# Performance work log

Hardware: AMD Instinct MI355X
Metric: run time of the kernel (lower is better)

## Reference

```python
import jax, jax.numpy as jnp
import numpy as np

NUM_HEADS = 12

def setup_inputs() -> dict:
    key = jax.random.key(0)
    k1, k2, k3 = jax.random.split(key, 3)
    B, N, C = 2, 4096, 768
    x = jax.random.normal(k1, (B, N, C), dtype=jnp.float32)
    w_qkv = jax.random.normal(k2, (C, 3 * C), dtype=jnp.float32) * 0.02
    b_qkv = jnp.zeros((3 * C,), dtype=jnp.float32)
    w_proj = jax.random.normal(k3, (C, C), dtype=jnp.float32) * 0.02
    b_proj = jnp.zeros((C,), dtype=jnp.float32)
    return {"x": x, "w_qkv": w_qkv, "b_qkv": b_qkv, "w_proj": w_proj, "b_proj": b_proj}

def reference(x, w_qkv, b_qkv, w_proj, b_proj):
    B, N, C = x.shape
    H = NUM_HEADS
    D = C // H
    # fused QKV projection: [B,N,3C] -> [B,N,3,H,D] -> [3,B,H,N,D]
    qkv = (x @ w_qkv + b_qkv).reshape(B, N, 3, H, D).transpose(2, 0, 3, 1, 4)
    q, k, v = qkv[0], qkv[1], qkv[2]
    # unnormalized (softmax-free) attention, same op order as the torch module
    attn = jnp.einsum('bhnd,bhmd->bhnm', q, k) / jnp.sqrt(jnp.float32(D))  # [B,H,N,N]
    out = jnp.einsum('bhnm,bhmd->bhnd', attn, v)  # [B,H,N,D]
    out = out.transpose(0, 2, 1, 3).reshape(B, N, C)
    return out @ w_proj + b_proj
```

## Files before the change

kernel.cpp:

```cpp
#include <hip/hip_runtime.h>

typedef unsigned short ushort_t;
typedef __bf16 bf16_t;
typedef __attribute__((ext_vector_type(8))) bf16_t bf16x8;
typedef __attribute__((ext_vector_type(4))) float f32x4;

__device__ __forceinline__ ushort_t f2bf(float f) {
  unsigned int u = __builtin_bit_cast(unsigned int, f);
  u += 0x7FFFu + ((u >> 16) & 1u);
  return (ushort_t)(u >> 16);
}

__device__ __forceinline__ float bf2f(ushort_t s) {
  return __builtin_bit_cast(float, (unsigned int)s << 16);
}

__device__ __forceinline__ f32x4 mfma16(bf16x8 a, bf16x8 b, f32x4 c) {
  return __builtin_amdgcn_mfma_f32_16x16x32_bf16(a, b, c, 0, 0, 0);
}

__device__ __forceinline__ void async_copy16(const void* g, void* l) {
  __builtin_amdgcn_global_load_lds(
      (const __attribute__((address_space(1))) unsigned int*)g,
      (__attribute__((address_space(3))) unsigned int*)l,
      16, 0, 0);
}

#define BARRIER { __builtin_amdgcn_s_barrier(); asm volatile("" ::: "memory"); }
#define VMW3 asm volatile("s_waitcnt vmcnt(3)" ::: "memory")
#define VMW0 asm volatile("s_waitcnt vmcnt(0)" ::: "memory")

__global__ __launch_bounds__(256) void conv_all_k(const float* __restrict__ x,
                                                  const float* __restrict__ w,
                                                  ushort_t* __restrict__ xb,
                                                  ushort_t* __restrict__ wqt,
                                                  ushort_t* __restrict__ wqr) {
  __shared__ float lds[64][65];
  const int bid = blockIdx.x;
  const int tid = threadIdx.x;
  if (bid < 3072) {
    int i = (bid * 256 + tid) * 8;
    float4 f0 = *(const float4*)(x + i);
    float4 f1 = *(const float4*)(x + i + 4);
    union { ushort_t s[8]; uint4 v; } u;
    u.s[0] = f2bf(f0.x); u.s[1] = f2bf(f0.y); u.s[2] = f2bf(f0.z); u.s[3] = f2bf(f0.w);
    u.s[4] = f2bf(f1.x); u.s[5] = f2bf(f1.y); u.s[6] = f2bf(f1.z); u.s[7] = f2bf(f1.w);
    *(uint4*)(xb + i) = u.v;
  } else if (bid < 3360) {
    const int ii = bid - 3072;
    const int n0 = 768 + (ii % 24) * 64;
    const int k0 = (ii / 24) * 64;
#pragma unroll
    for (int q = 0; q < 16; ++q) {
      int lin = tid + q * 256;
      int i = lin >> 6, j = lin & 63;
      lds[i][j] = w[(size_t)(k0 + i) * 2304 + n0 + j];
    }
    __syncthreads();
#pragma unroll
    for (int q = 0; q < 16; ++q) {
      int lin = tid + q * 256;
      int jj = lin >> 6, kk = lin & 63;
      wqt[(size_t)(n0 + jj) * 768 + k0 + kk] = f2bf(lds[kk][jj]);
    }
  } else {
    int i = ((bid - 3360) * 256 + tid) * 8;
    int row = i / 768, col = i % 768;
    const float* src = w + (size_t)row * 2304 + col;
    float4 f0 = *(const float4*)src;
    float4 f1 = *(const float4*)(src + 4);
    union { ushort_t s[8]; uint4 v; } u;
    u.s[0] = f2bf(f0.x); u.s[1] = f2bf(f0.y); u.s[2] = f2bf(f0.z); u.s[3] = f2bf(f0.w);
    u.s[4] = f2bf(f1.x); u.s[5] = f2bf(f1.y); u.s[6] = f2bf(f1.z); u.s[7] = f2bf(f1.w);
    *(uint4*)(wqr + i) = u.v;
  }
}

template <bool OUT_BF16>
__global__ __launch_bounds__(512, 2) void g256x192_k(
    const ushort_t* __restrict__ A, int lda, long long sA,
    const ushort_t* __restrict__ Bt, int ldb, long long sB,
    const float* __restrict__ bias, long long sBias,
    void* __restrict__ Cp, int ldc, long long sC,
    int K, int ntiles) {
  __shared__ char smem[114688];
  const int tid = threadIdx.x;
  const int lane = tid & 63;
  const int wid = tid >> 6;
  const int l15 = lane & 15, lhi = lane >> 4;
  const int wr = wid >> 2, wc = wid & 3;
  const int sx = l15 & 7;

  const int nwg = gridDim.x;
  const int q = nwg >> 3;
  const int swz = (blockIdx.x & 7) * q + (blockIdx.x >> 3);
  const int mt = swz / ntiles, nt = swz % ntiles;
  const int m0 = mt << 8, n0 = nt * 192;
  const long long z = blockIdx.y;

  const ushort_t* Ab = A + z * sA;
  const ushort_t* Bb = Bt + z * sB;

  const int r0 = tid >> 3;
  const int sg = tid & 7;
  const int soff = (sg ^ (r0 & 7)) << 4;

#define STAGE_A(BUF, H, K0)                                                      \
  { const char* g0 = (const char*)(Ab + (size_t)(m0 + (H)*128 + r0) * lda + (K0)) + soff;      \
    const char* g1 = (const char*)(Ab + (size_t)(m0 + (H)*128 + r0 + 64) * lda + (K0)) + soff; \
    char* lb = smem + (BUF)*57344 + (H)*16384;                                   \
    async_copy16(g0, lb + tid * 16);                                             \
    async_copy16(g1, lb + 8192 + tid * 16); }

#define STAGE_B3(BUF, J, K0)                                                     \
  { const char* g0 = (const char*)(Bb + (size_t)(n0 + (J)*64 + r0) * ldb + (K0)) + soff;       \
    async_copy16(g0, smem + (BUF)*57344 + 32768 + (J)*8192 + tid * 16); }

  const int aBase = wr * 16384 + l15 * 128;
  const int bBase = 32768 + (wc * 48 + l15) * 128;
  const int sk0 = ((lhi ^ sx) << 4);
  const int sk1 = (((4 + lhi) ^ sx) << 4);

  f32x4 acc[8][3] = {};
  bf16x8 bfr[3][2];

#define DS_A(BUF, MPAIR, AF)                                                     \
  _Pragma("unroll") for (int mm = 0; mm < 2; ++mm) {                             \
    AF[mm][0] = *(const bf16x8*)(smem + (BUF)*57344 + aBase + ((MPAIR)*2+mm)*2048 + sk0); \
    AF[mm][1] = *(const bf16x8*)(smem + (BUF)*57344 + aBase + ((MPAIR)*2+mm)*2048 + sk1); }

#define DS_B(BUF)                                                                \
  _Pragma("unroll") for (int n = 0; n < 3; ++n) {                                \
    bfr[n][0] = *(const bf16x8*)(smem + (BUF)*57344 + bBase + n*2048 + sk0);     \
    bfr[n][1] = *(const bf16x8*)(smem + (BUF)*57344 + bBase + n*2048 + sk1); }

#define MFMA_PH(MPAIR, AF)                                                       \
  __builtin_amdgcn_s_setprio(1);                                                 \
  _Pragma("unroll") for (int mm = 0; mm < 2; ++mm)                               \
    _Pragma("unroll") for (int n = 0; n < 3; ++n) {                              \
      acc[(MPAIR)*2+mm][n] = mfma16(AF[mm][0], bfr[n][0], acc[(MPAIR)*2+mm][n]); \
      acc[(MPAIR)*2+mm][n] = mfma16(AF[mm][1], bfr[n][1], acc[(MPAIR)*2+mm][n]); } \
  __builtin_amdgcn_s_setprio(0);

  STAGE_A(0, 0, 0) STAGE_A(0, 1, 0)
  STAGE_B3(0, 0, 0) STAGE_B3(0, 1, 0) STAGE_B3(0, 2, 0)
  STAGE_B3(1, 0, 64) STAGE_B3(1, 1, 64) STAGE_B3(1, 2, 64)
  VMW3;
  BARRIER

  const int NIT = K >> 7;
#pragma unroll 1
  for (int it = 0; it < NIT - 1; ++it) {
    const int kA = (it << 7) + 64;
    const int k2 = (it << 7) + 128;
    const int k3 = (it << 7) + 192;
    { bf16x8 af[2][2]; DS_B(0) DS_A(0, 0, af) STAGE_A(1, 0, kA)
      BARRIER MFMA_PH(0, af) BARRIER }
    { bf16x8 af[2][2]; DS_A(0, 1, af) STAGE_A(1, 1, kA)
      BARRIER MFMA_PH(1, af) BARRIER }
    { bf16x8 af[2][2]; DS_A(0, 2, af) STAGE_B3(0, 0, k2) STAGE_B3(0, 1, k2)
      BARRIER MFMA_PH(2, af) BARRIER }
    { bf16x8 af[2][2]; DS_A(0, 3, af) STAGE_B3(0, 2, k2) VMW3;
      BARRIER MFMA_PH(3, af) BARRIER }
    { bf16x8 af[2][2]; DS_B(1) DS_A(1, 0, af) STAGE_A(0, 0, k2)
      BARRIER MFMA_PH(0, af) BARRIER }
    { bf16x8 af[2][2]; DS_A(1, 1, af) STAGE_A(0, 1, k2)
      BARRIER MFMA_PH(1, af) BARRIER }
    { bf16x8 af[2][2]; DS_A(1, 2, af) STAGE_B3(1, 0, k3) STAGE_B3(1, 1, k3)
      BARRIER MFMA_PH(2, af) BARRIER }
    { bf16x8 af[2][2]; DS_A(1, 3, af) STAGE_B3(1, 2, k3) VMW3;
      BARRIER MFMA_PH(3, af) BARRIER }
  }
  {
    const int kA = ((NIT - 1) << 7) + 64;
    { bf16x8 af[2][2]; DS_B(0) DS_A(0, 0, af) STAGE_A(1, 0, kA)
      BARRIER MFMA_PH(0, af) BARRIER }
    { bf16x8 af[2][2]; DS_A(0, 1, af) STAGE_A(1, 1, kA)
      BARRIER MFMA_PH(1, af) BARRIER }
    { bf16x8 af[2][2]; DS_A(0, 2, af)
      BARRIER MFMA_PH(2, af) BARRIER }
    { bf16x8 af[2][2]; DS_A(0, 3, af) VMW0;
      BARRIER MFMA_PH(3, af) BARRIER }
    { bf16x8 af[2][2]; DS_B(1) DS_A(1, 0, af)
      BARRIER MFMA_PH(0, af) BARRIER }
    { bf16x8 af[2][2]; DS_A(1, 1, af)
      BARRIER MFMA_PH(1, af) BARRIER }
    { bf16x8 af[2][2]; DS_A(1, 2, af)
      BARRIER MFMA_PH(2, af) BARRIER }
    { bf16x8 af[2][2]; DS_A(1, 3, af)
      BARRIER MFMA_PH(3, af) BARRIER }
  }

  float bv[3];
#pragma unroll
  for (int n = 0; n < 3; ++n) bv[n] = bias[z * sBias + n0 + wc * 48 + n * 16 + l15];
#pragma unroll
  for (int m = 0; m < 8; ++m) {
#pragma unroll
    for (int n = 0; n < 3; ++n) {
#pragma unroll
      for (int ri = 0; ri < 4; ++ri) {
        int row = m0 + wr * 128 + m * 16 + lhi * 4 + ri;
        int col = n0 + wc * 48 + n * 16 + l15;
        float v = acc[m][n][ri] + bv[n];
        size_t ci = (size_t)z * sC + (size_t)row * ldc + col;
        if (OUT_BF16) ((ushort_t*)Cp)[ci] = f2bf(v);
        else          ((float*)Cp)[ci]    = v;
      }
    }
  }
#undef STAGE_A
#undef STAGE_B3
#undef DS_A
#undef DS_B
#undef MFMA_PH
}

template <bool OUT_BF16>
__global__ __launch_bounds__(512, 2) void g128x192_k(
    const ushort_t* __restrict__ A, int lda, long long sA,
    const ushort_t* __restrict__ Bt, int ldb, long long sB,
    const float* __restrict__ bias, long long sBias,
    void* __restrict__ Cp, int ldc, long long sC,
    int K, int ntiles) {
  __shared__ char smem[81920];
  const int tid = threadIdx.x;
  const int lane = tid & 63;
  const int wid = tid >> 6;
  const int l15 = lane & 15, lhi = lane >> 4;
  const int wr = wid >> 2, wc = wid & 3;
  const int sx = l15 & 7;

  const int nwg = gridDim.x;
  const int q = nwg >> 3;
  const int swz = (blockIdx.x & 7) * q + (blockIdx.x >> 3);
  const int mt = swz / ntiles, nt = swz % ntiles;
  const int m0 = mt << 7, n0 = nt * 192;
  const long long z = blockIdx.y;

  const ushort_t* Ab = A + z * sA;
  const ushort_t* Bb = Bt + z * sB;

  const int r0 = tid >> 3;
  const int sg = tid & 7;
  const int soff = (sg ^ (r0 & 7)) << 4;

#define STAGE_A1(BUF, K0)                                                        \
  { const char* g0 = (const char*)(Ab + (size_t)(m0 + r0) * lda + (K0)) + soff;               \
    const char* g1 = (const char*)(Ab + (size_t)(m0 + r0 + 64) * lda + (K0)) + soff;          \
    char* lb = smem + (BUF)*40960;                                               \
    async_copy16(g0, lb + tid * 16);                                             \
    async_copy16(g1, lb + 8192 + tid * 16); }

#define STAGE_B3(BUF, J, K0)                                                     \
  { const char* g0 = (const char*)(Bb + (size_t)(n0 + (J)*64 + r0) * ldb + (K0)) + soff;       \
    async_copy16(g0, smem + (BUF)*40960 + 16384 + (J)*8192 + tid * 16); }

  const int aBase = wr * 8192 + l15 * 128;
  const int bBase = 16384 + (wc * 48 + l15) * 128;
  const int sk0 = ((lhi ^ sx) << 4);
  const int sk1 = (((4 + lhi) ^ sx) << 4);

  f32x4 acc[4][3] = {};
  bf16x8 bfr[3][2];

#define DS_A1(BUF, M, AF)                                                        \
  { AF[0] = *(const bf16x8*)(smem + (BUF)*40960 + aBase + (M)*2048 + sk0);       \
    AF[1] = *(const bf16x8*)(smem + (BUF)*40960 + aBase + (M)*2048 + sk1); }

#define DS_B1(BUF)                                                               \
  _Pragma("unroll") for (int n = 0; n < 3; ++n) {                                \
    bfr[n][0] = *(const bf16x8*)(smem + (BUF)*40960 + bBase + n*2048 + sk0);     \
    bfr[n][1] = *(const bf16x8*)(smem + (BUF)*40960 + bBase + n*2048 + sk1); }

#define MFMA_PH1(M, AF)                                                          \
  __builtin_amdgcn_s_setprio(1);                                                 \
  _Pragma("unroll") for (int n = 0; n < 3; ++n) {                                \
    acc[M][n] = mfma16(AF[0], bfr[n][0], acc[M][n]);                             \
    acc[M][n] = mfma16(AF[1], bfr[n][1], acc[M][n]); }                           \
  __builtin_amdgcn_s_setprio(0);

  STAGE_A1(0, 0)
  STAGE_B3(0, 0, 0) STAGE_B3(0, 1, 0) STAGE_B3(0, 2, 0)
  STAGE_B3(1, 0, 64) STAGE_B3(1, 1, 64) STAGE_B3(1, 2, 64)
  VMW3;
  BARRIER

  const int NIT = K >> 7;
#pragma unroll 1
  for (int it = 0; it < NIT - 1; ++it) {
    const int kA = (it << 7) + 64;
    const int k2 = (it << 7) + 128;
    const int k3 = (it << 7) + 192;
    { bf16x8 af[2]; DS_B1(0) DS_A1(0, 0, af) STAGE_A1(1, kA)
      BARRIER MFMA_PH1(0, af) BARRIER }
    { bf16x8 af[2]; DS_A1(0, 1, af)
      BARRIER MFMA_PH1(1, af) BARRIER }
    { bf16x8 af[2]; DS_A1(0, 2, af) STAGE_B3(0, 0, k2) STAGE_B3(0, 1, k2)
      BARRIER MFMA_PH1(2, af) BARRIER }
    { bf16x8 af[2]; DS_A1(0, 3, af) STAGE_B3(0, 2, k2) VMW3;
      BARRIER MFMA_PH1(3, af) BARRIER }
    { bf16x8 af[2]; DS_B1(1) DS_A1(1, 0, af) STAGE_A1(0, k2)
      BARRIER MFMA_PH1(0, af) BARRIER }
    { bf16x8 af[2]; DS_A1(1, 1, af)
      BARRIER MFMA_PH1(1, af) BARRIER }
    { bf16x8 af[2]; DS_A1(1, 2, af) STAGE_B3(1, 0, k3) STAGE_B3(1, 1, k3)
      BARRIER MFMA_PH1(2, af) BARRIER }
    { bf16x8 af[2]; DS_A1(1, 3, af) STAGE_B3(1, 2, k3) VMW3;
      BARRIER MFMA_PH1(3, af) BARRIER }
  }
  {
    const int kA = ((NIT - 1) << 7) + 64;
    { bf16x8 af[2]; DS_B1(0) DS_A1(0, 0, af) STAGE_A1(1, kA)
      BARRIER MFMA_PH1(0, af) BARRIER }
    { bf16x8 af[2]; DS_A1(0, 1, af)
      BARRIER MFMA_PH1(1, af) BARRIER }
    { bf16x8 af[2]; DS_A1(0, 2, af)
      BARRIER MFMA_PH1(2, af) BARRIER }
    { bf16x8 af[2]; DS_A1(0, 3, af) VMW0;
      BARRIER MFMA_PH1(3, af) BARRIER }
    { bf16x8 af[2]; DS_B1(1) DS_A1(1, 0, af)
      BARRIER MFMA_PH1(0, af) BARRIER }
    { bf16x8 af[2]; DS_A1(1, 1, af)
      BARRIER MFMA_PH1(1, af) BARRIER }
    { bf16x8 af[2]; DS_A1(1, 2, af)
      BARRIER MFMA_PH1(2, af) BARRIER }
    { bf16x8 af[2]; DS_A1(1, 3, af)
      BARRIER MFMA_PH1(3, af) BARRIER }
  }

  float bv[3];
#pragma unroll
  for (int n = 0; n < 3; ++n) bv[n] = bias[z * sBias + n0 + wc * 48 + n * 16 + l15];
#pragma unroll
  for (int m = 0; m < 4; ++m) {
#pragma unroll
    for (int n = 0; n < 3; ++n) {
#pragma unroll
      for (int ri = 0; ri < 4; ++ri) {
        int row = m0 + wr * 64 + m * 16 + lhi * 4 + ri;
        int col = n0 + wc * 48 + n * 16 + l15;
        float v = acc[m][n][ri] + bv[n];
        size_t ci = (size_t)z * sC + (size_t)row * ldc + col;
        if (OUT_BF16) ((ushort_t*)Cp)[ci] = f2bf(v);
        else          ((float*)Cp)[ci]    = v;
      }
    }
  }
#undef STAGE_A1
#undef STAGE_B3
#undef DS_A1
#undef DS_B1
#undef MFMA_PH1
}

__global__ __launch_bounds__(256) void kv_k(const ushort_t* __restrict__ kv,
                                            float* __restrict__ Sp) {
  __shared__ ushort_t kt[64][34];
  __shared__ ushort_t vt[64][34];
  const int bh = blockIdx.x;
  const int chunk = blockIdx.y;
  const int b = bh / 12, h = bh % 12;
  const size_t base = (size_t)b * 4096 * 1536;
  const int koff = h * 64, voff = 768 + h * 64;
  const int tid = threadIdx.x;
  const int nn = tid >> 3;
  const int dg = (tid & 7) * 8;
  const int w = tid >> 6, l = tid & 63, l15 = l & 15, lhi = l >> 4;

  f32x4 acc[4] = {};
  const int nbeg = chunk * 256;
  for (int n0 = nbeg; n0 < nbeg + 256; n0 += 32) {
    __syncthreads();
    size_t rowb = base + (size_t)(n0 + nn) * 1536;
    union { uint4 v; ushort_t s[8]; } uk, uv;
    uk.v = *(const uint4*)(kv + rowb + koff + dg);
    uv.v = *(const uint4*)(kv + rowb + voff + dg);
#pragma unroll
    for (int j = 0; j < 8; ++j) {
      kt[dg + j][nn] = uk.s[j];
      vt[dg + j][nn] = uv.s[j];
    }
    __syncthreads();
    bf16x8 af = *(const bf16x8*)&kt[w * 16 + l15][lhi * 8];
#pragma unroll
    for (int t = 0; t < 4; ++t) {
      bf16x8 bf = *(const bf16x8*)&vt[t * 16 + l15][lhi * 8];
      acc[t] = mfma16(af, bf, acc[t]);
    }
  }
#pragma unroll
  for (int t = 0; t < 4; ++t) {
#pragma unroll
    for (int r = 0; r < 4; ++r) {
      int d1 = w * 16 + lhi * 4 + r;
      int d2 = t * 16 + l15;
      Sp[((size_t)chunk * 24 + bh) * 4096 + d1 * 64 + d2] = acc[t][r];
    }
  }
}

__global__ __launch_bounds__(256) void sred_k(const float* __restrict__ Sp,
                                              ushort_t* __restrict__ S) {
  int i = blockIdx.x * 256 + threadIdx.x;
  float a = 0.f;
#pragma unroll
  for (int c = 0; c < 16; ++c) a += Sp[(size_t)c * 98304 + i];
  S[i] = f2bf(a * 0.125f);
}

__global__ __launch_bounds__(256) void t_gemm_k(const ushort_t* __restrict__ S,
                                                const float* __restrict__ wproj,
                                                ushort_t* __restrict__ Tt) {
  __shared__ ushort_t a_lds[64][66];
  __shared__ ushort_t b_lds[64][66];
  const int n0 = blockIdx.x * 64;
  const int bh = blockIdx.y;
  const int b = bh / 12, h = bh % 12;
  const int tid = threadIdx.x;
  {
    int m = tid >> 2, kg = tid & 3;
#pragma unroll
    for (int j = 0; j < 16; ++j) {
      int k = kg * 16 + j;
      a_lds[m][k] = S[(size_t)bh * 4096 + m * 64 + k];
    }
    int n = tid & 63, kg2 = tid >> 6;
#pragma unroll
    for (int j = 0; j < 16; ++j) {
      int k = kg2 * 16 + j;
      b_lds[n][k] = f2bf(wproj[(size_t)(h * 64 + k) * 768 + n0 + n]);
    }
  }
  __syncthreads();
  const int w = tid >> 6, l = tid & 63, l15 = l & 15, lhi = l >> 4;
  f32x4 acc[4] = {};
#pragma unroll
  for (int kk = 0; kk < 64; kk += 32) {
    bf16x8 af = *(const bf16x8*)&a_lds[w * 16 + l15][kk + lhi * 8];
#pragma unroll
    for (int t = 0; t < 4; ++t) {
      bf16x8 bf = *(const bf16x8*)&b_lds[t * 16 + l15][kk + lhi * 8];
      acc[t] = mfma16(af, bf, acc[t]);
    }
  }
#pragma unroll
  for (int t = 0; t < 4; ++t) {
#pragma unroll
    for (int r = 0; r < 4; ++r) {
      int row = h * 64 + w * 16 + lhi * 4 + r;
      int col = n0 + t * 16 + l15;
      Tt[(size_t)b * 768 * 768 + (size_t)col * 768 + row] = f2bf(acc[t][r]);
    }
  }
}

__global__ __launch_bounds__(256) void ugcv_k(const ushort_t* __restrict__ Tt,
                                              const ushort_t* __restrict__ wqr,
                                              const float* __restrict__ bq,
                                              const float* __restrict__ bproj,
                                              ushort_t* __restrict__ Ut,
                                              float* __restrict__ cvec) {
  __shared__ ushort_t a_lds[64][72];
  __shared__ ushort_t b_lds[64][72];
  const int bid = blockIdx.x;
  const int tid = threadIdx.x;
  if (bid < 288) {
    const int n0 = (bid % 12) * 64, m0 = ((bid / 12) % 12) * 64;
    const long long z = bid / 144;
    const ushort_t* Ab = Tt + z * 768 * 768;
    const int w = tid >> 6, l = tid & 63, l15 = l & 15, lhi = l >> 4;
    const int r2 = tid >> 3, kc = (tid & 7) * 8;
    f32x4 acc[4] = {};
    for (int k0 = 0; k0 < 768; k0 += 64) {
      __syncthreads();
      *(uint4*)&a_lds[r2][kc]      = *(const uint4*)(Ab + (size_t)(m0 + r2) * 768 + k0 + kc);
      *(uint4*)&a_lds[r2 + 32][kc] = *(const uint4*)(Ab + (size_t)(m0 + r2 + 32) * 768 + k0 + kc);
      *(uint4*)&b_lds[r2][kc]      = *(const uint4*)(wqr + (size_t)(n0 + r2) * 768 + k0 + kc);
      *(uint4*)&b_lds[r2 + 32][kc] = *(const uint4*)(wqr + (size_t)(n0 + r2 + 32) * 768 + k0 + kc);
      __syncthreads();
#pragma unroll
      for (int kk = 0; kk < 2; ++kk) {
        bf16x8 af = *(const bf16x8*)&a_lds[w * 16 + l15][kk * 32 + lhi * 8];
#pragma unroll
        for (int t = 0; t < 4; ++t) {
          bf16x8 bf = *(const bf16x8*)&b_lds[t * 16 + l15][kk * 32 + lhi * 8];
          acc[t] = mfma16(af, bf, acc[t]);
        }
      }
    }
#pragma unroll
    for (int t = 0; t < 4; ++t) {
#pragma unroll
      for (int r = 0; r < 4; ++r) {
        int row = m0 + w * 16 + lhi * 4 + r, col = n0 + t * 16 + l15;
        Ut[z * 768 * 768 + (size_t)row * 768 + col] = f2bf(acc[t][r]);
      }
    }
  } else {
    const int row = (bid - 288) * 4 + (tid >> 6);
    const int lane = tid & 63;
    const ushort_t* r = Tt + (size_t)row * 768;
    float acc = 0.f;
#pragma unroll
    for (int k0 = 0; k0 < 768; k0 += 256) {
      int k = k0 + lane * 4;
      float4 b4 = *(const float4*)(bq + k);
      union { unsigned long long v; ushort_t s[4]; } u;
      u.v = *(const unsigned long long*)(r + k);
      acc += b4.x * bf2f(u.s[0]) + b4.y * bf2f(u.s[1]) +
             b4.z * bf2f(u.s[2]) + b4.w * bf2f(u.s[3]);
    }
#pragma unroll
    for (int off = 32; off > 0; off >>= 1) acc += __shfl_down(acc, off, 64);
    if (lane == 0) cvec[row] = acc + bproj[row % 768];
  }
}

extern "C" void kernel_launch(void* const* d_in, const int* in_sizes, int n_in,
                              void* d_out, int out_size, void* d_ws, size_t ws_size,
                              hipStream_t stream) {
  const float* x      = (const float*)d_in[0];
  const float* w_qkv  = (const float*)d_in[1];
  const float* b_qkv  = (const float*)d_in[2];
  const float* w_proj = (const float*)d_in[3];
  const float* b_proj = (const float*)d_in[4];
  float* out = (float*)d_out;

  char* ws = (char*)d_ws;
  ushort_t* xb   = (ushort_t*)ws;
  ushort_t* wqt  = (ushort_t*)(ws + 12582912);
  ushort_t* wqr  = (ushort_t*)(ws + 16121856);
  ushort_t* Ut   = (ushort_t*)(ws + 17301504);
  ushort_t* kv   = (ushort_t*)(ws + 19660800);
  float*    Sp   = (float*)   (ws + 44826624);
  ushort_t* S    = (ushort_t*)(ws + 51118080);
  ushort_t* Tt   = (ushort_t*)(ws + 51314688);
  float*    cvec = (float*)   (ws + 53673984);

  conv_all_k<<<dim3(3648), 256, 0, stream>>>(x, w_qkv, xb, wqt, wqr);
  g256x192_k<true><<<dim3(256, 1), 512, 0, stream>>>(
      xb, 768, 0LL, wqt + 768 * 768, 768, 0LL, b_qkv + 768, 0LL,
      kv, 1536, 0LL, 768, 8);
  kv_k<<<dim3(24, 16), 256, 0, stream>>>(kv, Sp);
  sred_k<<<dim3(384), 256, 0, stream>>>(Sp, S);
  t_gemm_k<<<dim3(12, 24), 256, 0, stream>>>(S, w_proj, Tt);
  ugcv_k<<<dim3(672), 256, 0, stream>>>(Tt, wqr, b_qkv, b_proj, Ut, cvec);
  g128x192_k<false><<<dim3(128, 2), 512, 0, stream>>>(
      xb, 768, 4096LL * 768, Ut, 768, 768LL * 768, cvec, 768LL,
      out, 768, 4096LL * 768, 768, 4);
}
```

Measured before the change: 78.45 us.

## Fuse four small tail kernels into one persistent kernel with grid barriers

Replaces the kv_k, sred_k, t_gemm_k and ugcv_k launches with a single 512-block tail kernel. An atomic-counter grid barrier separates the phases, which removes the launch gaps between the small kernels. The K^T V partial sums now use 8 chunks of 512 rows instead of 16 chunks of 256, so each block does more work and the reduction is shorter. The cost is an extra memset, spin-wait barriers that assume all 512 blocks are resident at once (deadlock risk otherwise), and less parallelism in the first phase.

```diff
diff --git a/kernel.cpp b/kernel.cpp
--- a/kernel.cpp
+++ b/kernel.cpp
@@ -29,6 +29,17 @@
 #define BARRIER { __builtin_amdgcn_s_barrier(); asm volatile("" ::: "memory"); }
 #define VMW3 asm volatile("s_waitcnt vmcnt(3)" ::: "memory")
 #define VMW0 asm volatile("s_waitcnt vmcnt(0)" ::: "memory")
+
+__device__ __forceinline__ void gsync(unsigned* cnt, unsigned want) {
+  __syncthreads();
+  if (threadIdx.x == 0) {
+    __threadfence();
+    atomicAdd(cnt, 1u);
+    while (atomicAdd(cnt, 0u) < want) __builtin_amdgcn_s_sleep(8);
+  }
+  __syncthreads();
+  __threadfence();
+}
 
 __global__ __launch_bounds__(256) void conv_all_k(const float* __restrict__ x,
                                                   const float* __restrict__ w,
@@ -354,166 +365,160 @@
 #undef MFMA_PH1
 }
 
-__global__ __launch_bounds__(256) void kv_k(const ushort_t* __restrict__ kv,
-                                            float* __restrict__ Sp) {
-  __shared__ ushort_t kt[64][34];
-  __shared__ ushort_t vt[64][34];
-  const int bh = blockIdx.x;
-  const int chunk = blockIdx.y;
-  const int b = bh / 12, h = bh % 12;
-  const size_t base = (size_t)b * 4096 * 1536;
-  const int koff = h * 64, voff = 768 + h * 64;
-  const int tid = threadIdx.x;
-  const int nn = tid >> 3;
-  const int dg = (tid & 7) * 8;
-  const int w = tid >> 6, l = tid & 63, l15 = l & 15, lhi = l >> 4;
-
-  f32x4 acc[4] = {};
-  const int nbeg = chunk * 256;
-  for (int n0 = nbeg; n0 < nbeg + 256; n0 += 32) {
-    __syncthreads();
-    size_t rowb = base + (size_t)(n0 + nn) * 1536;
-    union { uint4 v; ushort_t s[8]; } uk, uv;
-    uk.v = *(const uint4*)(kv + rowb + koff + dg);
-    uv.v = *(const uint4*)(kv + rowb + voff + dg);
-#pragma unroll
-    for (int j = 0; j < 8; ++j) {
-      kt[dg + j][nn] = uk.s[j];
-      vt[dg + j][nn] = uv.s[j];
-    }
-    __syncthreads();
-    bf16x8 af = *(const bf16x8*)&kt[w * 16 + l15][lhi * 8];
-#pragma unroll
-    for (int t = 0; t < 4; ++t) {
-      bf16x8 bf = *(const bf16x8*)&vt[t * 16 + l15][lhi * 8];
-      acc[t] = mfma16(af, bf, acc[t]);
-    }
-  }
-#pragma unroll
-  for (int t = 0; t < 4; ++t) {
-#pragma unroll
-    for (int r = 0; r < 4; ++r) {
-      int d1 = w * 16 + lhi * 4 + r;
-      int d2 = t * 16 + l15;
-      Sp[((size_t)chunk * 24 + bh) * 4096 + d1 * 64 + d2] = acc[t][r];
-    }
-  }
-}
-
-__global__ __launch_bounds__(256) void sred_k(const float* __restrict__ Sp,
-                                              ushort_t* __restrict__ S) {
-  int i = blockIdx.x * 256 + threadIdx.x;
-  float a = 0.f;
-#pragma unroll
-  for (int c = 0; c < 16; ++c) a += Sp[(size_t)c * 98304 + i];
-  S[i] = f2bf(a * 0.125f);
-}
-
-__global__ __launch_bounds__(256) void t_gemm_k(const ushort_t* __restrict__ S,
-                                                const float* __restrict__ wproj,
-                                                ushort_t* __restrict__ Tt) {
-  __shared__ ushort_t a_lds[64][66];
-  __shared__ ushort_t b_lds[64][66];
-  const int n0 = blockIdx.x * 64;
-  const int bh = blockIdx.y;
-  const int b = bh / 12, h = bh % 12;
-  const int tid = threadIdx.x;
-  {
-    int m = tid >> 2, kg = tid & 3;
-#pragma unroll
-    for (int j = 0; j < 16; ++j) {
-      int k = kg * 16 + j;
-      a_lds[m][k] = S[(size_t)bh * 4096 + m * 64 + k];
-    }
-    int n = tid & 63, kg2 = tid >> 6;
-#pragma unroll
-    for (int j = 0; j < 16; ++j) {
-      int k = kg2 * 16 + j;
-      b_lds[n][k] = f2bf(wproj[(size_t)(h * 64 + k) * 768 + n0 + n]);
-    }
-  }
-  __syncthreads();
-  const int w = tid >> 6, l = tid & 63, l15 = l & 15, lhi = l >> 4;
-  f32x4 acc[4] = {};
-#pragma unroll
-  for (int kk = 0; kk < 64; kk += 32) {
-    bf16x8 af = *(const bf16x8*)&a_lds[w * 16 + l15][kk + lhi * 8];
-#pragma unroll
-    for (int t = 0; t < 4; ++t) {
-      bf16x8 bf = *(const bf16x8*)&b_lds[t * 16 + l15][kk + lhi * 8];
-      acc[t] = mfma16(af, bf, acc[t]);
-    }
-  }
-#pragma unroll
-  for (int t = 0; t < 4; ++t) {
-#pragma unroll
-    for (int r = 0; r < 4; ++r) {
-      int row = h * 64 + w * 16 + lhi * 4 + r;
-      int col = n0 + t * 16 + l15;
-      Tt[(size_t)b * 768 * 768 + (size_t)col * 768 + row] = f2bf(acc[t][r]);
-    }
-  }
-}
-
-__global__ __launch_bounds__(256) void ugcv_k(const ushort_t* __restrict__ Tt,
-                                              const ushort_t* __restrict__ wqr,
-                                              const float* __restrict__ bq,
-                                              const float* __restrict__ bproj,
-                                              ushort_t* __restrict__ Ut,
-                                              float* __restrict__ cvec) {
-  __shared__ ushort_t a_lds[64][72];
-  __shared__ ushort_t b_lds[64][72];
+__global__ __launch_bounds__(256) void tail_k(
+    const ushort_t* __restrict__ kv, float* __restrict__ Sp,
+    ushort_t* __restrict__ S, const float* __restrict__ wproj,
+    ushort_t* __restrict__ Tt, const ushort_t* __restrict__ wqr,
+    const float* __restrict__ bq, const float* __restrict__ bproj,
+    ushort_t* __restrict__ Ut, float* __restrict__ cvec,
+    unsigned* __restrict__ cnt) {
+  __shared__ ushort_t sm[9216];
   const int bid = blockIdx.x;
   const int tid = threadIdx.x;
+
+  if (bid < 192) {
+    const int bh = bid % 24, chunk = bid / 24;
+    const int b = bh / 12, h = bh % 12;
+    const size_t base = (size_t)b * 4096 * 1536;
+    const int koff = h * 64, voff = 768 + h * 64;
+    const int nn = tid >> 3;
+    const int dg = (tid & 7) * 8;
+    const int w = tid >> 6, l15 = tid & 15, lhi = (tid & 63) >> 4;
+    ushort_t* kt = sm;
+    ushort_t* vt = sm + 64 * 34;
+    f32x4 acc[4] = {};
+    const int nbeg = chunk * 512;
+    for (int n0 = nbeg; n0 < nbeg + 512; n0 += 32) {
+      __syncthreads();
+      size_t rowb = base + (size_t)(n0 + nn) * 1536;
+      union { uint4 v; ushort_t s[8]; } uk, uv;
+      uk.v = *(const uint4*)(kv + rowb + koff + dg);
+      uv.v = *(const uint4*)(kv + rowb + voff + dg);
+#pragma unroll
+      for (int j = 0; j < 8; ++j) {
+        kt[(dg + j) * 34 + nn] = uk.s[j];
+        vt[(dg + j) * 34 + nn] = uv.s[j];
+      }
+      __syncthreads();
+      bf16x8 af = *(const bf16x8*)&kt[(w * 16 + l15) * 34 + lhi * 8];
+#pragma unroll
+      for (int t = 0; t < 4; ++t) {
+        bf16x8 bf = *(const bf16x8*)&vt[(t * 16 + l15) * 34 + lhi * 8];
+        acc[t] = mfma16(af, bf, acc[t]);
+      }
+    }
+#pragma unroll
+    for (int t = 0; t < 4; ++t)
+#pragma unroll
+      for (int r = 0; r < 4; ++r)
+        Sp[((size_t)chunk * 24 + bh) * 4096 +
+           (w * 16 + lhi * 4 + r) * 64 + t * 16 + l15] = acc[t][r];
+  }
+  gsync(cnt, 512);
+
+  if (bid < 384) {
+    int i = bid * 256 + tid;
+    float a = 0.f;
+#pragma unroll
+    for (int c = 0; c < 8; ++c) a += Sp[(size_t)c * 98304 + i];
+    S[i] = f2bf(a * 0.125f);
+  }
+  gsync(cnt, 1024);
+
+  if (bid < 288) {
+    const int n0 = (bid % 12) * 64;
+    const int bh = bid / 12;
+    const int b = bh / 12, h = bh % 12;
+    ushort_t* a_lds = sm;
+    ushort_t* b_lds = sm + 64 * 66;
+    {
+      int m = tid >> 2, kg = tid & 3;
+#pragma unroll
+      for (int j = 0; j < 16; ++j) {
+        int k = kg * 16 + j;
+        a_lds[m * 66 + k] = S[(size_t)bh * 4096 + m * 64 + k];
+      }
+      int n = tid & 63, kg2 = tid >> 6;
+#pragma unroll
+      for (int j = 0; j < 16; ++j) {
+        int k = kg2 * 16 + j;
+        b_lds[n * 66 + k] = f2bf(wproj[(size_t)(h * 64 + k) * 768 + n0 + n]);
+      }
+    }
+    __syncthreads();
+    const int w = tid >> 6, l = tid & 63, l15 = l & 15, lhi = l >> 4;
+    f32x4 acc[4] = {};
+#pragma unroll
+    for (int kk = 0; kk < 64; kk += 32) {
+      bf16x8 af = *(const bf16x8*)&a_lds[(w * 16 + l15) * 66 + kk + lhi * 8];
+#pragma unroll
+      for (int t = 0; t < 4; ++t) {
+        bf16x8 bf = *(const bf16x8*)&b_lds[(t * 16 + l15) * 66 + kk + lhi * 8];
+        acc[t] = mfma16(af, bf, acc[t]);
+      }
+    }
+#pragma unroll
+    for (int t = 0; t < 4; ++t)
+#pragma unroll
+      for (int r = 0; r < 4; ++r) {
+        int row = h * 64 + w * 16 + lhi * 4 + r;
+        int col = n0 + t * 16 + l15;
+        Tt[(size_t)b * 768 * 768 + (size_t)col * 768 + row] = f2bf(acc[t][r]);
+      }
+  }
+  gsync(cnt, 1536);
+
   if (bid < 288) {
     const int n0 = (bid % 12) * 64, m0 = ((bid / 12) % 12) * 64;
     const long long z = bid / 144;
     const ushort_t* Ab = Tt + z * 768 * 768;
+    ushort_t* a_lds = sm;
+    ushort_t* b_lds = sm + 64 * 72;
     const int w = tid >> 6, l = tid & 63, l15 = l & 15, lhi = l >> 4;
     const int r2 = tid >> 3, kc = (tid & 7) * 8;
     f32x4 acc[4] = {};
     for (int k0 = 0; k0 < 768; k0 += 64) {
       __syncthreads();
-      *(uint4*)&a_lds[r2][kc]      = *(const uint4*)(Ab + (size_t)(m0 + r2) * 768 + k0 + kc);
-      *(uint4*)&a_lds[r2 + 32][kc] = *(const uint4*)(Ab + (size_t)(m0 + r2 + 32) * 768 + k0 + kc);
-      *(uint4*)&b_lds[r2][kc]      = *(const uint4*)(wqr + (size_t)(n0 + r2) * 768 + k0 + kc);
-      *(uint4*)&b_lds[r2 + 32][kc] = *(const uint4*)(wqr + (size_t)(n0 + r2 + 32) * 768 + k0 + kc);
+      *(uint4*)&a_lds[r2 * 72 + kc]        = *(const uint4*)(Ab + (size_t)(m0 + r2) * 768 + k0 + kc);
+      *(uint4*)&a_lds[(r2 + 32) * 72 + kc] = *(const uint4*)(Ab + (size_t)(m0 + r2 + 32) * 768 + k0 + kc);
+      *(uint4*)&b_lds[r2 * 72 + kc]        = *(const uint4*)(wqr + (size_t)(n0 + r2) * 768 + k0 + kc);
+      *(uint4*)&b_lds[(r2 + 32) * 72 + kc] = *(const uint4*)(wqr + (size_t)(n0 + r2 + 32) * 768 + k0 + kc);
       __syncthreads();
 #pragma unroll
       for (int kk = 0; kk < 2; ++kk) {
-        bf16x8 af = *(const bf16x8*)&a_lds[w * 16 + l15][kk * 32 + lhi * 8];
+        bf16x8 af = *(const bf16x8*)&a_lds[(w * 16 + l15) * 72 + kk * 32 + lhi * 8];
 #pragma unroll
         for (int t = 0; t < 4; ++t) {
-          bf16x8 bf = *(const bf16x8*)&b_lds[t * 16 + l15][kk * 32 + lhi * 8];
+          bf16x8 bf = *(const bf16x8*)&b_lds[(t * 16 + l15) * 72 + kk * 32 + lhi * 8];
           acc[t] = mfma16(af, bf, acc[t]);
         }
       }
     }
 #pragma unroll
-    for (int t = 0; t < 4; ++t) {
+    for (int t = 0; t < 4; ++t)
 #pragma unroll
       for (int r = 0; r < 4; ++r) {
         int row = m0 + w * 16 + lhi * 4 + r, col = n0 + t * 16 + l15;
         Ut[z * 768 * 768 + (size_t)row * 768 + col] = f2bf(acc[t][r]);
       }
-    }
   } else {
-    const int row = (bid - 288) * 4 + (tid >> 6);
     const int lane = tid & 63;
-    const ushort_t* r = Tt + (size_t)row * 768;
-    float acc = 0.f;
-#pragma unroll
-    for (int k0 = 0; k0 < 768; k0 += 256) {
-      int k = k0 + lane * 4;
-      float4 b4 = *(const float4*)(bq + k);
-      union { unsigned long long v; ushort_t s[4]; } u;
-      u.v = *(const unsigned long long*)(r + k);
-      acc += b4.x * bf2f(u.s[0]) + b4.y * bf2f(u.s[1]) +
-             b4.z * bf2f(u.s[2]) + b4.w * bf2f(u.s[3]);
-    }
-#pragma unroll
-    for (int off = 32; off > 0; off >>= 1) acc += __shfl_down(acc, off, 64);
-    if (lane == 0) cvec[row] = acc + bproj[row % 768];
+    for (int row = (bid - 288) * 4 + (tid >> 6); row < 1536; row += 224 * 4) {
+      const ushort_t* r = Tt + (size_t)row * 768;
+      float acc = 0.f;
+#pragma unroll
+      for (int k0 = 0; k0 < 768; k0 += 256) {
+        int k = k0 + lane * 4;
+        float4 b4 = *(const float4*)(bq + k);
+        union { unsigned long long v; ushort_t s[4]; } u;
+        u.v = *(const unsigned long long*)(r + k);
+        acc += b4.x * bf2f(u.s[0]) + b4.y * bf2f(u.s[1]) +
+               b4.z * bf2f(u.s[2]) + b4.w * bf2f(u.s[3]);
+      }
+#pragma unroll
+      for (int off = 32; off > 0; off >>= 1) acc += __shfl_down(acc, off, 64);
+      if (lane == 0) cvec[row] = acc + bproj[row % 768];
+    }
   }
 }
 
@@ -537,15 +542,15 @@
   ushort_t* S    = (ushort_t*)(ws + 51118080);
   ushort_t* Tt   = (ushort_t*)(ws + 51314688);
   float*    cvec = (float*)   (ws + 53673984);
+  unsigned* cnt  = (unsigned*)(ws + 53680128);
 
   conv_all_k<<<dim3(3648), 256, 0, stream>>>(x, w_qkv, xb, wqt, wqr);
   g256x192_k<true><<<dim3(256, 1), 512, 0, stream>>>(
       xb, 768, 0LL, wqt + 768 * 768, 768, 0LL, b_qkv + 768, 0LL,
       kv, 1536, 0LL, 768, 8);
-  kv_k<<<dim3(24, 16), 256, 0, stream>>>(kv, Sp);
-  sred_k<<<dim3(384), 256, 0, stream>>>(Sp, S);
-  t_gemm_k<<<dim3(12, 24), 256, 0, stream>>>(S, w_proj, Tt);
-  ugcv_k<<<dim3(672), 256, 0, stream>>>(Tt, wqr, b_qkv, b_proj, Ut, cvec);
+  hipMemsetAsync(cnt, 0, 4, stream);
+  tail_k<<<dim3(512), 256, 0, stream>>>(kv, Sp, S, w_proj, Tt, wqr,
+                                        b_qkv, b_proj, Ut, cvec, cnt);
   g128x192_k<false><<<dim3(128, 2), 512, 0, stream>>>(
       xb, 768, 4096LL * 768, Ut, 768, 768LL * 768, cvec, 768LL,
       out, 768, 4096LL * 768, 768, 4);
```

New measurement: 280.3 us. 3.57x slower.
